# Kernel optimization log

Hardware: AMD Instinct MI355X
Metric: run time of the kernel (lower is better)

The kernel has to match this reference:

```python
import jax, jax.numpy as jnp
import numpy as np

B, S, I, H = 32, 1024, 512, 512


def setup_inputs() -> dict:
    key = jax.random.key(0)
    ks = jax.random.split(key, 5)
    scale_ih = 1.0 / np.sqrt(I)
    scale_hh = 1.0 / np.sqrt(H)
    return {
        "x": jax.random.normal(ks[0], (B, S, I), dtype=jnp.float32),
        "W_ih": jax.random.normal(ks[1], (4 * H, I), dtype=jnp.float32) * scale_ih,
        "W_hh": jax.random.normal(ks[2], (4 * H, H), dtype=jnp.float32) * scale_hh,
        "b_ih": jax.random.normal(ks[3], (4 * H,), dtype=jnp.float32) * scale_hh,
        "b_hh": jax.random.normal(ks[4], (4 * H,), dtype=jnp.float32) * scale_hh,
        "h0": jnp.zeros((B, H), dtype=jnp.float32),
        "c0": jnp.zeros((B, H), dtype=jnp.float32),
    }


def reference(x, W_ih, W_hh, b_ih, b_hh, h0, c0):
    # Precompute input contribution for all timesteps: [B, S, 4H]
    x_gates = jnp.einsum('bsi,gi->bsg', x, W_ih) + b_ih + b_hh

    def step(carry, xg_t):
        h, c = carry
        gates = xg_t + h @ W_hh.T  # [B, 4H]
        i_g, f_g, g_g, o_g = jnp.split(gates, 4, axis=-1)
        i_g = jax.nn.sigmoid(i_g)
        f_g = jax.nn.sigmoid(f_g)
        g_g = jnp.tanh(g_g)
        o_g = jax.nn.sigmoid(o_g)
        c_new = f_g * c + i_g * g_g
        h_new = o_g * jnp.tanh(c_new)
        return (h_new, c_new), h_new

    # scan over time: [S, B, 4H]
    (h_n, c_n), ys = jax.lax.scan(step, (h0, c0), jnp.swapaxes(x_gates, 0, 1))
    output = jnp.swapaxes(ys, 0, 1)  # [B, S, H]
    return output, h_n, c_n
```

## Files before the change

kernel.cpp:

```cpp
#include <hip/hip_runtime.h>
#include <stdint.h>


typedef __attribute__((ext_vector_type(8))) short bf16x8;
typedef __attribute__((ext_vector_type(4))) float f32x4;

__device__ __forceinline__ unsigned short f2bf(float f) {
  union { float f; unsigned u; } v; v.f = f;
  unsigned r = (v.u + 0x7fffu + ((v.u >> 16) & 1u)) >> 16;
  return (unsigned short)r;
}
__device__ __forceinline__ float bf2f(unsigned short h) {
  union { unsigned u; float f; } v; v.u = ((unsigned)h) << 16;
  return v.f;
}

__global__ __launch_bounds__(256) void cvt_bf16(const float* __restrict__ in,
                                                unsigned short* __restrict__ out, int n) {
  int i = (blockIdx.x * 256 + threadIdx.x) * 4;
  if (i >= n) return;
  float4 v = *(const float4*)(in + i);
  ushort4 o;
  o.x = f2bf(v.x); o.y = f2bf(v.y); o.z = f2bf(v.z); o.w = f2bf(v.w);
  *(ushort4*)(out + i) = o;
}

__global__ __launch_bounds__(256) void gemm_xg(const unsigned short* __restrict__ A,
                                               const unsigned short* __restrict__ Bw,
                                               const float* __restrict__ b_ih,
                                               const float* __restrict__ b_hh,
                                               unsigned short* __restrict__ xg) {
  __shared__ unsigned short Asub[128][32];
  __shared__ unsigned short Bsub[128][32];
  const int tid = threadIdx.x;
  const int mb = blockIdx.x >> 4;
  const int nb = blockIdx.x & 15;
  const int wv = tid >> 6, ln = tid & 63;
  const int wr = wv >> 1, wc = wv & 1;
  const int lrow = tid >> 1;
  const int lseg = (tid & 1) * 16;

  const unsigned short* Ag = A + (size_t)(mb * 128 + lrow) * 512 + lseg;
  const unsigned short* Bg = Bw + (size_t)(nb * 128 + lrow) * 512 + lseg;

  f32x4 acc[4][4] = {};
  const int frow = ln & 15;
  const int kq = (ln >> 4) * 8;

  for (int k0 = 0; k0 < 512; k0 += 32) {
    uint4 a0 = *(const uint4*)(Ag + k0);
    uint4 a1 = *(const uint4*)(Ag + k0 + 8);
    uint4 b0 = *(const uint4*)(Bg + k0);
    uint4 b1 = *(const uint4*)(Bg + k0 + 8);
    __syncthreads();
    *(uint4*)&Asub[lrow][lseg]     = a0;
    *(uint4*)&Asub[lrow][lseg + 8] = a1;
    *(uint4*)&Bsub[lrow][lseg]     = b0;
    *(uint4*)&Bsub[lrow][lseg + 8] = b1;
    __syncthreads();
    bf16x8 af[4], bfr[4];
#pragma unroll
    for (int mi = 0; mi < 4; ++mi)
      af[mi] = *(const bf16x8*)&Asub[wr * 64 + mi * 16 + frow][kq];
#pragma unroll
    for (int ni = 0; ni < 4; ++ni)
      bfr[ni] = *(const bf16x8*)&Bsub[wc * 64 + ni * 16 + frow][kq];
#pragma unroll
    for (int mi = 0; mi < 4; ++mi)
#pragma unroll
      for (int ni = 0; ni < 4; ++ni)
        acc[mi][ni] = __builtin_amdgcn_mfma_f32_16x16x32_bf16(af[mi], bfr[ni], acc[mi][ni], 0, 0, 0);
  }

  const int col0 = nb * 128 + wc * 64 + frow;
  float bias[4];
#pragma unroll
  for (int ni = 0; ni < 4; ++ni)
    bias[ni] = b_ih[col0 + ni * 16] + b_hh[col0 + ni * 16];

#pragma unroll
  for (int mi = 0; mi < 4; ++mi) {
    const int m0 = mb * 128 + wr * 64 + mi * 16 + (ln >> 4) * 4;
#pragma unroll
    for (int ni = 0; ni < 4; ++ni) {
#pragma unroll
      for (int rr = 0; rr < 4; ++rr) {
        float v = acc[mi][ni][rr] + bias[ni];
        xg[(size_t)(m0 + rr) * 2048 + col0 + ni * 16] = f2bf(v);
      }
    }
  }
}

#define ROW_FMA(A, W0v, W1v, W2v, W3v)                                        \
  A = fmaf(W0v.x, hv0.x, A); A = fmaf(W0v.y, hv0.y, A);                       \
  A = fmaf(W0v.z, hv0.z, A); A = fmaf(W0v.w, hv0.w, A);                       \
  A = fmaf(W1v.x, hv1.x, A); A = fmaf(W1v.y, hv1.y, A);                       \
  A = fmaf(W1v.z, hv1.z, A); A = fmaf(W1v.w, hv1.w, A);                       \
  A = fmaf(W2v.x, hv2.x, A); A = fmaf(W2v.y, hv2.y, A);                       \
  A = fmaf(W2v.z, hv2.z, A); A = fmaf(W2v.w, hv2.w, A);                       \
  A = fmaf(W3v.x, hv3.x, A); A = fmaf(W3v.y, hv3.y, A);                       \
  A = fmaf(W3v.z, hv3.z, A); A = fmaf(W3v.w, hv3.w, A)

#define FMA_BATCH(b)                                                          \
  do {                                                                        \
    f32x4 hv0 = *(const f32x4*)&h_lds[(b) * 512 + kcb16];                     \
    f32x4 hv1 = *(const f32x4*)&h_lds[(b) * 512 + kcb16 + 4];                 \
    f32x4 hv2 = *(const f32x4*)&h_lds[(b) * 512 + kcb16 + 8];                 \
    f32x4 hv3 = *(const f32x4*)&h_lds[(b) * 512 + kcb16 + 12];                \
    ROW_FMA(acc[0][b], Wr0_0, Wr0_1, Wr0_2, Wr0_3);                           \
    ROW_FMA(acc[1][b], Wr1_0, Wr1_1, Wr1_2, Wr1_3);                           \
    ROW_FMA(acc[2][b], Wr2_0, Wr2_1, Wr2_2, Wr2_3);                           \
    ROW_FMA(acc[3][b], Wr3_0, Wr3_1, Wr3_2, Wr3_3);                           \
  } while (0)

__global__ __launch_bounds__(512, 1) void lstm_rec(const unsigned short* __restrict__ xg,
                                                   const float* __restrict__ W_hh,
                                                   const float* __restrict__ h0,
                                                   const float* __restrict__ c0,
                                                   float* __restrict__ out,
                                                   float* __restrict__ hn,
                                                   float* __restrict__ cn,
                                                   float* h_buf,
                                                   unsigned int* flags) {
  __shared__ float h_lds[2048];
  __shared__ float scratch[8704];
  __shared__ float c_lds[64];

  const int tid = threadIdx.x;
  const int g = blockIdx.x & 7;
  const int w = blockIdx.x >> 3;
  const int gb0 = g * 4;
  const int kc = tid >> 4;
  const int rg = tid & 15;
  const int kcb16 = kc * 16;
  unsigned int* gflags = flags + g * 1024;

  const int grow0 = (rg >> 2) * 512 + w * 16 + (rg & 3) * 4;
  const float* wp0 = W_hh + (size_t)(grow0 + 0) * 512 + kcb16;
  const float* wp1 = W_hh + (size_t)(grow0 + 1) * 512 + kcb16;
  const float* wp2 = W_hh + (size_t)(grow0 + 2) * 512 + kcb16;
  const float* wp3 = W_hh + (size_t)(grow0 + 3) * 512 + kcb16;
  f32x4 Wr0_0 = *(const f32x4*)(wp0), Wr0_1 = *(const f32x4*)(wp0 + 4),
        Wr0_2 = *(const f32x4*)(wp0 + 8), Wr0_3 = *(const f32x4*)(wp0 + 12);
  f32x4 Wr1_0 = *(const f32x4*)(wp1), Wr1_1 = *(const f32x4*)(wp1 + 4),
        Wr1_2 = *(const f32x4*)(wp1 + 8), Wr1_3 = *(const f32x4*)(wp1 + 12);
  f32x4 Wr2_0 = *(const f32x4*)(wp2), Wr2_1 = *(const f32x4*)(wp2 + 4),
        Wr2_2 = *(const f32x4*)(wp2 + 8), Wr2_3 = *(const f32x4*)(wp2 + 12);
  f32x4 Wr3_0 = *(const f32x4*)(wp3), Wr3_1 = *(const f32x4*)(wp3 + 4),
        Wr3_2 = *(const f32x4*)(wp3 + 8), Wr3_3 = *(const f32x4*)(wp3 + 12);
  asm volatile("" : "+v"(Wr0_0), "+v"(Wr0_1), "+v"(Wr0_2), "+v"(Wr0_3),
                    "+v"(Wr1_0), "+v"(Wr1_1), "+v"(Wr1_2), "+v"(Wr1_3),
                    "+v"(Wr2_0), "+v"(Wr2_1), "+v"(Wr2_2), "+v"(Wr2_3),
                    "+v"(Wr3_0), "+v"(Wr3_1), "+v"(Wr3_2), "+v"(Wr3_3));

  {
    *(float4*)&h_lds[tid * 4] = *(const float4*)(h0 + gb0 * 512 + tid * 4);
    if (tid < 64) {
      int jj = tid & 15, bb = tid >> 4;
      c_lds[bb * 16 + jj] = c0[(gb0 + bb) * 512 + w * 16 + jj];
    }
  }
  __syncthreads();

  const int lane = tid & 63;
  const int b2 = tid >> 6;
  const int jj = lane & 15;
  const int grow_r = (lane >> 4) * 512 + w * 16 + jj;

  for (int t = 0; t < 1024; ++t) {
    float xg_v = 0.f;
    if (tid < 256)
      xg_v = bf2f(xg[(size_t)((gb0 + b2) * 1024 + t) * 2048 + grow_r]);

    float acc[4][4] = {};
    FMA_BATCH(0); FMA_BATCH(1); FMA_BATCH(2); FMA_BATCH(3);

#pragma unroll
    for (int b = 0; b < 4; ++b) {
      f32x4 v;
      v.x = acc[0][b]; v.y = acc[1][b]; v.z = acc[2][b]; v.w = acc[3][b];
      *(f32x4*)&scratch[b * 2176 + kc * 68 + rg * 4] = v;
    }
    __syncthreads();

    if (tid < 256) {
      const float* sp = &scratch[b2 * 2176 + lane];
      float s0 = 0.f, s1 = 0.f, s2 = 0.f, s3 = 0.f;
#pragma unroll
      for (int q = 0; q < 32; q += 4) {
        s0 += sp[q * 68];
        s1 += sp[(q + 1) * 68];
        s2 += sp[(q + 2) * 68];
        s3 += sp[(q + 3) * 68];
      }
      float s = xg_v + ((s0 + s1) + (s2 + s3));
      float gi = __shfl(s, jj);
      float gf = __shfl(s, jj + 16);
      float gc = __shfl(s, jj + 32);
      float go = __shfl(s, jj + 48);
      if (lane < 16) {
        float ig = 1.f / (1.f + __expf(-gi));
        float fg = 1.f / (1.f + __expf(-gf));
        float gt = tanhf(gc);
        float og = 1.f / (1.f + __expf(-go));
        float c = fmaf(fg, c_lds[b2 * 16 + jj], ig * gt);
        c_lds[b2 * 16 + jj] = c;
        float hv = og * tanhf(c);
        out[(size_t)((gb0 + b2) * 1024 + t) * 512 + w * 16 + jj] = hv;
        __hip_atomic_store(&h_buf[((t + 1) & 1) * 16384 + (gb0 + b2) * 512 + w * 16 + jj], hv,
                           __ATOMIC_RELAXED, __HIP_MEMORY_SCOPE_AGENT);
        if (t == 1023) {
          hn[(gb0 + b2) * 512 + w * 16 + jj] = hv;
          cn[(gb0 + b2) * 512 + w * 16 + jj] = c;
        }
      }
    }
    __syncthreads();

    if (t < 1023) {
      if (tid == 0)
        __hip_atomic_store(&gflags[w * 32], (unsigned)(t + 1),
                           __ATOMIC_RELAXED, __HIP_MEMORY_SCOPE_AGENT);
      const unsigned target = (unsigned)(t + 1);
      for (;;) {
        unsigned f = target;
        if (lane < 32)
          f = __hip_atomic_load(&gflags[lane * 32], __ATOMIC_RELAXED,
                                __HIP_MEMORY_SCOPE_AGENT);
        if (__all(f >= target)) break;
        __builtin_amdgcn_s_sleep(1);
      }
      asm volatile("" ::: "memory");
      const unsigned long long* hb =
          (const unsigned long long*)(h_buf + ((t + 1) & 1) * 16384 + gb0 * 512 + tid * 4);
      unsigned long long v0 = __hip_atomic_load(hb,     __ATOMIC_RELAXED, __HIP_MEMORY_SCOPE_AGENT);
      unsigned long long v1 = __hip_atomic_load(hb + 1, __ATOMIC_RELAXED, __HIP_MEMORY_SCOPE_AGENT);
      *(unsigned long long*)&h_lds[tid * 4]     = v0;
      *(unsigned long long*)&h_lds[tid * 4 + 2] = v1;
      __syncthreads();
    }
  }
}

extern "C" void kernel_launch(void* const* d_in, const int* in_sizes, int n_in,
                              void* d_out, int out_size, void* d_ws, size_t ws_size,
                              hipStream_t stream) {
  const float* x    = (const float*)d_in[0];
  const float* W_ih = (const float*)d_in[1];
  const float* W_hh = (const float*)d_in[2];
  const float* b_ih = (const float*)d_in[3];
  const float* b_hh = (const float*)d_in[4];
  const float* h0   = (const float*)d_in[5];
  const float* c0   = (const float*)d_in[6];
  float* out = (float*)d_out;
  float* hn = out + (size_t)32 * 1024 * 512;
  float* cn = hn + 32 * 512;

  uint8_t* ws = (uint8_t*)d_ws;
  unsigned short* xg   = (unsigned short*)ws;
  unsigned short* x_bf = (unsigned short*)(ws + 134217728u);
  unsigned short* w_bf = (unsigned short*)(ws + 167772160u);
  float* h_buf         = (float*)(ws + 169869312u);
  unsigned int* flags  = (unsigned int*)(ws + 170000384u);

  hipMemsetAsync(flags, 0, 8 * 4096, stream);
  cvt_bf16<<<dim3(16384), dim3(256), 0, stream>>>(x, x_bf, 16777216);
  cvt_bf16<<<dim3(1024), dim3(256), 0, stream>>>(W_ih, w_bf, 1048576);
  gemm_xg<<<dim3(4096), dim3(256), 0, stream>>>(x_bf, w_bf, b_ih, b_hh, xg);

  void* args[] = {(void*)&xg, (void*)&W_hh, (void*)&h0, (void*)&c0,
                  (void*)&out, (void*)&hn, (void*)&cn, (void*)&h_buf, (void*)&flags};
  hipLaunchCooperativeKernel((const void*)lstm_rec, dim3(256), dim3(512), args, 0, stream);
}
```

Before: 3.319 ms.

## Replace flag barrier with sentinel-tagged 4-slot hidden-state exchange

Drops the per-step flag counters and the extra block barrier. Consumers now spin directly on the hidden-state values in a 4-slot ring buffer, and each producer resets the slot two steps back to a NaN sentinel pattern. This removes a store-flag, load-flags and reload round trip from every recurrent step, which sits on the serial critical path. In exchange it depends on a real h value never matching the sentinel bits and on the ordering of relaxed atomics across slots, and it adds a memset of the buffer.

After: 4.090 ms. +23.2%, slower.

```diff
diff --git a/kernel.cpp b/kernel.cpp
--- a/kernel.cpp
+++ b/kernel.cpp
@@ -114,6 +114,8 @@
     ROW_FMA(acc[3][b], Wr3_0, Wr3_1, Wr3_2, Wr3_3);                           \
   } while (0)
 
+#define SENT 0xFFFFFFFFu
+
 __global__ __launch_bounds__(512, 1) void lstm_rec(const unsigned short* __restrict__ xg,
                                                    const float* __restrict__ W_hh,
                                                    const float* __restrict__ h0,
@@ -121,8 +123,7 @@
                                                    float* __restrict__ out,
                                                    float* __restrict__ hn,
                                                    float* __restrict__ cn,
-                                                   float* h_buf,
-                                                   unsigned int* flags) {
+                                                   float* h_buf) {
   __shared__ float h_lds[2048];
   __shared__ float scratch[8704];
   __shared__ float c_lds[64];
@@ -134,7 +135,6 @@
   const int kc = tid >> 4;
   const int rg = tid & 15;
   const int kcb16 = kc * 16;
-  unsigned int* gflags = flags + g * 1024;
 
   const int grow0 = (rg >> 2) * 512 + w * 16 + (rg & 3) * 4;
   const float* wp0 = W_hh + (size_t)(grow0 + 0) * 512 + kcb16;
@@ -184,6 +184,9 @@
     }
     __syncthreads();
 
+    const int slot = (t + 1) & 3;
+    float* hslot = h_buf + slot * 16384;
+
     if (tid < 256) {
       const float* sp = &scratch[b2 * 2176 + lane];
       float s0 = 0.f, s1 = 0.f, s2 = 0.f, s3 = 0.f;
@@ -207,35 +210,31 @@
         float c = fmaf(fg, c_lds[b2 * 16 + jj], ig * gt);
         c_lds[b2 * 16 + jj] = c;
         float hv = og * tanhf(c);
+        const int hidx = (gb0 + b2) * 512 + w * 16 + jj;
+        __hip_atomic_store(&hslot[hidx], hv,
+                           __ATOMIC_RELAXED, __HIP_MEMORY_SCOPE_AGENT);
+        __hip_atomic_store((unsigned*)&h_buf[((t + 3) & 3) * 16384 + hidx], SENT,
+                           __ATOMIC_RELAXED, __HIP_MEMORY_SCOPE_AGENT);
         out[(size_t)((gb0 + b2) * 1024 + t) * 512 + w * 16 + jj] = hv;
-        __hip_atomic_store(&h_buf[((t + 1) & 1) * 16384 + (gb0 + b2) * 512 + w * 16 + jj], hv,
-                           __ATOMIC_RELAXED, __HIP_MEMORY_SCOPE_AGENT);
         if (t == 1023) {
-          hn[(gb0 + b2) * 512 + w * 16 + jj] = hv;
-          cn[(gb0 + b2) * 512 + w * 16 + jj] = c;
+          hn[hidx] = hv;
+          cn[hidx] = c;
         }
       }
     }
-    __syncthreads();
 
     if (t < 1023) {
-      if (tid == 0)
-        __hip_atomic_store(&gflags[w * 32], (unsigned)(t + 1),
-                           __ATOMIC_RELAXED, __HIP_MEMORY_SCOPE_AGENT);
-      const unsigned target = (unsigned)(t + 1);
+      const unsigned long long* hb =
+          (const unsigned long long*)(hslot + gb0 * 512 + tid * 4);
+      unsigned long long v0, v1;
       for (;;) {
-        unsigned f = target;
-        if (lane < 32)
-          f = __hip_atomic_load(&gflags[lane * 32], __ATOMIC_RELAXED,
-                                __HIP_MEMORY_SCOPE_AGENT);
-        if (__all(f >= target)) break;
+        v0 = __hip_atomic_load(hb,     __ATOMIC_RELAXED, __HIP_MEMORY_SCOPE_AGENT);
+        v1 = __hip_atomic_load(hb + 1, __ATOMIC_RELAXED, __HIP_MEMORY_SCOPE_AGENT);
+        if ((unsigned)v0 != SENT && (unsigned)(v0 >> 32) != SENT &&
+            (unsigned)v1 != SENT && (unsigned)(v1 >> 32) != SENT)
+          break;
         __builtin_amdgcn_s_sleep(1);
       }
-      asm volatile("" ::: "memory");
-      const unsigned long long* hb =
-          (const unsigned long long*)(h_buf + ((t + 1) & 1) * 16384 + gb0 * 512 + tid * 4);
-      unsigned long long v0 = __hip_atomic_load(hb,     __ATOMIC_RELAXED, __HIP_MEMORY_SCOPE_AGENT);
-      unsigned long long v1 = __hip_atomic_load(hb + 1, __ATOMIC_RELAXED, __HIP_MEMORY_SCOPE_AGENT);
       *(unsigned long long*)&h_lds[tid * 4]     = v0;
       *(unsigned long long*)&h_lds[tid * 4 + 2] = v1;
       __syncthreads();
@@ -262,14 +261,13 @@
   unsigned short* x_bf = (unsigned short*)(ws + 134217728u);
   unsigned short* w_bf = (unsigned short*)(ws + 167772160u);
   float* h_buf         = (float*)(ws + 169869312u);
-  unsigned int* flags  = (unsigned int*)(ws + 170000384u);
-
-  hipMemsetAsync(flags, 0, 8 * 4096, stream);
+
+  hipMemsetAsync(h_buf, 0xFF, 262144, stream);
   cvt_bf16<<<dim3(16384), dim3(256), 0, stream>>>(x, x_bf, 16777216);
   cvt_bf16<<<dim3(1024), dim3(256), 0, stream>>>(W_ih, w_bf, 1048576);
   gemm_xg<<<dim3(4096), dim3(256), 0, stream>>>(x_bf, w_bf, b_ih, b_hh, xg);
 
   void* args[] = {(void*)&xg, (void*)&W_hh, (void*)&h0, (void*)&c0,
-                  (void*)&out, (void*)&hn, (void*)&cn, (void*)&h_buf, (void*)&flags};
+                  (void*)&out, (void*)&hn, (void*)&cn, (void*)&h_buf};
   hipLaunchCooperativeKernel((const void*)lstm_rec, dim3(256), dim3(512), args, 0, stream);
 }
```
